# Kernel optimization log

Measured on AMD Instinct MI355X. Metric: run time of the kernel, lower is better.

Reference implementation:

```python
import jax, jax.numpy as jnp
import numpy as np

K, R, D = 200000, 64, 1024
N_IDS = 16384
BITS = 4
GROUP = 32


def group_quantize(w, bits, group_size):
    """Group-wise symmetric fake-quant along the last dim (STE in bwd)."""
    last = w.shape[-1]
    g = min(group_size, last)
    n_groups = last // g
    wg = w.reshape(w.shape[:-1] + (n_groups, g))
    amax = jnp.clip(jnp.max(jnp.abs(wg), axis=-1, keepdims=True), 1e-8, None)
    q_max = (1 << (bits - 1)) - 1  # matches torch `1 << bits - 1` precedence
    scale = amax / q_max
    q = jnp.clip(jnp.round(wg / scale), -q_max, q_max) * scale
    # straight-through estimator: forward = q, backward = identity w.r.t. wg
    wq = wg + jax.lax.stop_gradient(q - wg)
    return wq.reshape(w.shape)


def setup_inputs() -> dict:
    key = jax.random.key(0)
    k1, k2, k3 = jax.random.split(key, 3)
    U = jax.random.normal(k1, (K, R), dtype=jnp.float32)
    B = jax.random.normal(k2, (R, D), dtype=jnp.float32)
    local_ids = jax.random.randint(k3, (N_IDS,), 0, K, dtype=jnp.int64 if jax.config.read('jax_enable_x64') else jnp.int32)
    return {"U": U, "B": B, "local_ids": local_ids}


def reference(U, B, local_ids):
    # row(): quantize ALL of U, gather selected rows, matmul with quantized B
    Uq = group_quantize(U, BITS, min(GROUP, R))   # [K, r]
    Bq = group_quantize(B, BITS, min(GROUP, D))   # [r, d]
    return Uq[local_ids] @ Bq                      # [N, d]
```

## Files before the change

kernel.cpp:

```cpp
#include <hip/hip_runtime.h>


#define R_DIM 64
#define D_DIM 1024
#define N_IDS 16384

#define BM 64
#define BN 128
#define LDS_STRIDE 72
#define OT_STRIDE 132

typedef __attribute__((ext_vector_type(8))) __bf16 bf16x8;
typedef __attribute__((ext_vector_type(4))) float f32x4;

__device__ inline unsigned short f32_to_bf16_rne(float f) {
  union { float f; unsigned int u; } c; c.f = f;
  unsigned int u = c.u;
  u += 0x7fffu + ((u >> 16) & 1u);
  return (unsigned short)(u >> 16);
}

__device__ inline float bf16_bits_to_f32(unsigned short h) {
  union { unsigned int u; float f; } c; c.u = ((unsigned int)h) << 16;
  return c.f;
}

__device__ inline void quant_split(float w, float a, unsigned short* hi, unsigned short* lo) {
  double amax  = fmax((double)a, 1e-8);
  double scale = amax / 7.0;
  double t     = (double)w / scale;
  double q     = fmin(fmax(rint(t), -7.0), 7.0) * scale;
  float qf = (float)q;
  unsigned short h = f32_to_bf16_rne(qf);
  *hi = h;
  *lo = f32_to_bf16_rne(qf - bf16_bits_to_f32(h));
}

__global__ __launch_bounds__(256) void quantB_kernel(
    const float* __restrict__ B,
    unsigned short* __restrict__ BqT_hi, unsigned short* __restrict__ BqT_lo) {
  int e = blockIdx.x * 256 + threadIdx.x;
  int r = e >> 10;
  int c = e & 1023;
  float w = B[e];
  float a = fabsf(w);
  a = fmaxf(a, __shfl_xor(a, 1));
  a = fmaxf(a, __shfl_xor(a, 2));
  a = fmaxf(a, __shfl_xor(a, 4));
  a = fmaxf(a, __shfl_xor(a, 8));
  a = fmaxf(a, __shfl_xor(a, 16));
  unsigned short hi, lo;
  quant_split(w, a, &hi, &lo);
  BqT_hi[c * R_DIM + r] = hi;
  BqT_lo[c * R_DIM + r] = lo;
}

__global__ __launch_bounds__(256) void gemm_kernel(
    const float* __restrict__ U, const int* __restrict__ ids,
    const unsigned short* __restrict__ BqT_hi, const unsigned short* __restrict__ BqT_lo,
    float* __restrict__ out) {
  __shared__ char smem[2 * BN * LDS_STRIDE * 2];
  unsigned short* bt_hi = (unsigned short*)smem;
  unsigned short* bt_lo = bt_hi + BN * LDS_STRIDE;
  float* ot = (float*)smem;

  const int tid  = threadIdx.x;
  const int lane = tid & 63;
  const int wave = tid >> 6;
  const int bx   = blockIdx.x;
  const int nb   = bx & 7;
  const int mb   = bx >> 3;
  const int n0   = nb * BN;

  {
    const uint4* src_hi = (const uint4*)(BqT_hi + (size_t)n0 * R_DIM);
    const uint4* src_lo = (const uint4*)(BqT_lo + (size_t)n0 * R_DIM);
    #pragma unroll
    for (int it = 0; it < 4; ++it) {
      int c = tid + it * 256;
      int row = c >> 3, off = c & 7;
      *(uint4*)&bt_hi[row * LDS_STRIDE + off * 8] = src_hi[c];
      *(uint4*)&bt_lo[row * LDS_STRIDE + off * 8] = src_lo[c];
    }
  }

  const int m0    = mb * BM + wave * 16;
  const int rowid = ids[m0 + (lane & 15)];
  const int koff  = (lane >> 4) * 8;
  const int nlane = lane & 15;
  const float* urow = U + (size_t)rowid * R_DIM;

  bf16x8 afrag_hi[2], afrag_lo[2];
  #pragma unroll
  for (int s = 0; s < 2; ++s) {
    float4 w0 = *(const float4*)(urow + s * 32 + koff);
    float4 w1 = *(const float4*)(urow + s * 32 + koff + 4);
    float wv[8] = {w0.x, w0.y, w0.z, w0.w, w1.x, w1.y, w1.z, w1.w};
    float a = 0.0f;
    #pragma unroll
    for (int j = 0; j < 8; ++j) a = fmaxf(a, fabsf(wv[j]));
    a = fmaxf(a, __shfl_xor(a, 16));
    a = fmaxf(a, __shfl_xor(a, 32));
    union { unsigned short s8[8]; bf16x8 b; } uh, ul;
    #pragma unroll
    for (int j = 0; j < 8; ++j) {
      unsigned short hi, lo;
      quant_split(wv[j], a, &hi, &lo);
      uh.s8[j] = hi;
      ul.s8[j] = lo;
    }
    afrag_hi[s] = uh.b;
    afrag_lo[s] = ul.b;
  }

  __syncthreads();

  f32x4 acc[8];
  #pragma unroll
  for (int nf = 0; nf < 8; ++nf) acc[nf] = (f32x4){0.f, 0.f, 0.f, 0.f};

  #pragma unroll
  for (int nf = 0; nf < 8; ++nf) {
    #pragma unroll
    for (int s = 0; s < 2; ++s) {
      const int boff = (nf * 16 + nlane) * LDS_STRIDE + s * 32 + koff;
      union { uint4 u; bf16x8 b; } bh, bl;
      bh.u = *(const uint4*)&bt_hi[boff];
      bl.u = *(const uint4*)&bt_lo[boff];
      acc[nf] = __builtin_amdgcn_mfma_f32_16x16x32_bf16(afrag_hi[s], bh.b, acc[nf], 0, 0, 0);
      acc[nf] = __builtin_amdgcn_mfma_f32_16x16x32_bf16(afrag_hi[s], bl.b, acc[nf], 0, 0, 0);
      acc[nf] = __builtin_amdgcn_mfma_f32_16x16x32_bf16(afrag_lo[s], bh.b, acc[nf], 0, 0, 0);
    }
  }

  __syncthreads();

  float* w = ot + wave * 16 * OT_STRIDE;
  {
    const int r0 = (lane >> 4) << 2;
    #pragma unroll
    for (int nf = 0; nf < 8; ++nf) {
      #pragma unroll
      for (int i = 0; i < 4; ++i) {
        w[(r0 + i) * OT_STRIDE + nlane + nf * 16] = acc[nf][i];
      }
    }
  }
  #pragma unroll
  for (int j = 0; j < 8; ++j) {
    const int row = j * 2 + (lane >> 5);
    f32x4 v = *(const f32x4*)&w[row * OT_STRIDE + (lane & 31) * 4];
    __builtin_nontemporal_store(v,
        (f32x4*)&out[(size_t)(m0 + row) * D_DIM + n0 + (lane & 31) * 4]);
  }
}

extern "C" void kernel_launch(void* const* d_in, const int* in_sizes, int n_in,
                              void* d_out, int out_size, void* d_ws, size_t ws_size,
                              hipStream_t stream) {
  const float* U   = (const float*)d_in[0];
  const float* B   = (const float*)d_in[1];
  const int*   ids = (const int*)d_in[2];
  float* out = (float*)d_out;

  unsigned short* BqT_hi = (unsigned short*)d_ws;
  unsigned short* BqT_lo = BqT_hi + R_DIM * D_DIM;

  quantB_kernel<<<(R_DIM * D_DIM) / 256, 256, 0, stream>>>(B, BqT_hi, BqT_lo);
  gemm_kernel<<<(N_IDS / BM) * (D_DIM / BN), 256, 0, stream>>>(U, ids, BqT_hi, BqT_lo, out);
}
```

Baseline: 27.29 us.

## Double GEMM M-tile per block, hoist gathered U loads, vectorize B quantization

Each gemm block now covers 128 rows instead of 64, and each wave computes two 16-row fragments. That way every B fragment read from LDS feeds twice as many MFMAs, and the per-block B tile staging is amortized over more output rows. The gathered U row loads are issued before the B tile is copied into LDS, so their global latency overlaps the staging. quantB now processes four elements per thread with a float4 load and shorter shuffle reductions, and the gemm kernel gets a launch-bounds occupancy hint. The trade-off is higher register pressure and half as many blocks in the grid, which could reduce latency hiding in a kernel that is mostly bound by output writes.

```diff
diff --git a/kernel.cpp b/kernel.cpp
--- a/kernel.cpp
+++ b/kernel.cpp
@@ -5,7 +5,7 @@
 #define D_DIM 1024
 #define N_IDS 16384
 
-#define BM 64
+#define BM 128
 #define BN 128
 #define LDS_STRIDE 72
 #define OT_STRIDE 132
@@ -25,11 +25,10 @@
   return c.f;
 }
 
-__device__ inline void quant_split(float w, float a, unsigned short* hi, unsigned short* lo) {
-  double amax  = fmax((double)a, 1e-8);
-  double scale = amax / 7.0;
-  double t     = (double)w / scale;
-  double q     = fmin(fmax(rint(t), -7.0), 7.0) * scale;
+__device__ inline void quant_elem(float w, double scale,
+                                  unsigned short* hi, unsigned short* lo) {
+  double t = (double)w / scale;
+  double q = fmin(fmax(rint(t), -7.0), 7.0) * scale;
   float qf = (float)q;
   unsigned short h = f32_to_bf16_rne(qf);
   *hi = h;
@@ -39,23 +38,27 @@
 __global__ __launch_bounds__(256) void quantB_kernel(
     const float* __restrict__ B,
     unsigned short* __restrict__ BqT_hi, unsigned short* __restrict__ BqT_lo) {
-  int e = blockIdx.x * 256 + threadIdx.x;
-  int r = e >> 10;
-  int c = e & 1023;
-  float w = B[e];
-  float a = fabsf(w);
+  int e4 = blockIdx.x * 256 + threadIdx.x;
+  int e  = e4 * 4;
+  int r  = e >> 10;
+  int c  = e & 1023;
+  float4 w = *(const float4*)(B + e);
+  float a = fmaxf(fmaxf(fabsf(w.x), fabsf(w.y)), fmaxf(fabsf(w.z), fabsf(w.w)));
   a = fmaxf(a, __shfl_xor(a, 1));
   a = fmaxf(a, __shfl_xor(a, 2));
   a = fmaxf(a, __shfl_xor(a, 4));
-  a = fmaxf(a, __shfl_xor(a, 8));
-  a = fmaxf(a, __shfl_xor(a, 16));
-  unsigned short hi, lo;
-  quant_split(w, a, &hi, &lo);
-  BqT_hi[c * R_DIM + r] = hi;
-  BqT_lo[c * R_DIM + r] = lo;
+  double sc = fmax((double)a, 1e-8) / 7.0;
+  float wv[4] = {w.x, w.y, w.z, w.w};
+  #pragma unroll
+  for (int j = 0; j < 4; ++j) {
+    unsigned short hi, lo;
+    quant_elem(wv[j], sc, &hi, &lo);
+    BqT_hi[(c + j) * R_DIM + r] = hi;
+    BqT_lo[(c + j) * R_DIM + r] = lo;
+  }
 }
 
-__global__ __launch_bounds__(256) void gemm_kernel(
+__global__ __launch_bounds__(256, 4) void gemm_kernel(
     const float* __restrict__ U, const int* __restrict__ ids,
     const unsigned short* __restrict__ BqT_hi, const unsigned short* __restrict__ BqT_lo,
     float* __restrict__ out) {
@@ -71,6 +74,20 @@
   const int nb   = bx & 7;
   const int mb   = bx >> 3;
   const int n0   = nb * BN;
+  const int m0b  = mb * BM;
+  const int koff  = (lane >> 4) * 8;
+  const int nlane = lane & 15;
+
+  const float* urow0 = U + (size_t)ids[m0b + wave * 16 + nlane] * R_DIM;
+  const float* urow1 = U + (size_t)ids[m0b + 64 + wave * 16 + nlane] * R_DIM;
+  float4 wr[2][2][2];
+  #pragma unroll
+  for (int s = 0; s < 2; ++s) {
+    wr[0][s][0] = *(const float4*)(urow0 + s * 32 + koff);
+    wr[0][s][1] = *(const float4*)(urow0 + s * 32 + koff + 4);
+    wr[1][s][0] = *(const float4*)(urow1 + s * 32 + koff);
+    wr[1][s][1] = *(const float4*)(urow1 + s * 32 + koff + 4);
+  }
 
   {
     const uint4* src_hi = (const uint4*)(BqT_hi + (size_t)n0 * R_DIM);
@@ -84,40 +101,39 @@
     }
   }
 
-  const int m0    = mb * BM + wave * 16;
-  const int rowid = ids[m0 + (lane & 15)];
-  const int koff  = (lane >> 4) * 8;
-  const int nlane = lane & 15;
-  const float* urow = U + (size_t)rowid * R_DIM;
-
-  bf16x8 afrag_hi[2], afrag_lo[2];
+  bf16x8 ah[2][2], al[2][2];
   #pragma unroll
-  for (int s = 0; s < 2; ++s) {
-    float4 w0 = *(const float4*)(urow + s * 32 + koff);
-    float4 w1 = *(const float4*)(urow + s * 32 + koff + 4);
-    float wv[8] = {w0.x, w0.y, w0.z, w0.w, w1.x, w1.y, w1.z, w1.w};
-    float a = 0.0f;
+  for (int mf = 0; mf < 2; ++mf) {
     #pragma unroll
-    for (int j = 0; j < 8; ++j) a = fmaxf(a, fabsf(wv[j]));
-    a = fmaxf(a, __shfl_xor(a, 16));
-    a = fmaxf(a, __shfl_xor(a, 32));
-    union { unsigned short s8[8]; bf16x8 b; } uh, ul;
-    #pragma unroll
-    for (int j = 0; j < 8; ++j) {
-      unsigned short hi, lo;
-      quant_split(wv[j], a, &hi, &lo);
-      uh.s8[j] = hi;
-      ul.s8[j] = lo;
+    for (int s = 0; s < 2; ++s) {
+      float4 w0 = wr[mf][s][0], w1 = wr[mf][s][1];
+      float wv[8] = {w0.x, w0.y, w0.z, w0.w, w1.x, w1.y, w1.z, w1.w};
+      float a = 0.0f;
+      #pragma unroll
+      for (int j = 0; j < 8; ++j) a = fmaxf(a, fabsf(wv[j]));
+      a = fmaxf(a, __shfl_xor(a, 16));
+      a = fmaxf(a, __shfl_xor(a, 32));
+      double sc = fmax((double)a, 1e-8) / 7.0;
+      union { unsigned short s8[8]; bf16x8 b; } uh, ul;
+      #pragma unroll
+      for (int j = 0; j < 8; ++j) {
+        unsigned short hi, lo;
+        quant_elem(wv[j], sc, &hi, &lo);
+        uh.s8[j] = hi;
+        ul.s8[j] = lo;
+      }
+      ah[mf][s] = uh.b;
+      al[mf][s] = ul.b;
     }
-    afrag_hi[s] = uh.b;
-    afrag_lo[s] = ul.b;
   }
 
   __syncthreads();
 
-  f32x4 acc[8];
+  f32x4 acc[2][8];
   #pragma unroll
-  for (int nf = 0; nf < 8; ++nf) acc[nf] = (f32x4){0.f, 0.f, 0.f, 0.f};
+  for (int mf = 0; mf < 2; ++mf)
+    #pragma unroll
+    for (int nf = 0; nf < 8; ++nf) acc[mf][nf] = (f32x4){0.f, 0.f, 0.f, 0.f};
 
   #pragma unroll
   for (int nf = 0; nf < 8; ++nf) {
@@ -127,31 +143,36 @@
       union { uint4 u; bf16x8 b; } bh, bl;
       bh.u = *(const uint4*)&bt_hi[boff];
       bl.u = *(const uint4*)&bt_lo[boff];
-      acc[nf] = __builtin_amdgcn_mfma_f32_16x16x32_bf16(afrag_hi[s], bh.b, acc[nf], 0, 0, 0);
-      acc[nf] = __builtin_amdgcn_mfma_f32_16x16x32_bf16(afrag_hi[s], bl.b, acc[nf], 0, 0, 0);
-      acc[nf] = __builtin_amdgcn_mfma_f32_16x16x32_bf16(afrag_lo[s], bh.b, acc[nf], 0, 0, 0);
+      #pragma unroll
+      for (int mf = 0; mf < 2; ++mf) {
+        acc[mf][nf] = __builtin_amdgcn_mfma_f32_16x16x32_bf16(ah[mf][s], bh.b, acc[mf][nf], 0, 0, 0);
+        acc[mf][nf] = __builtin_amdgcn_mfma_f32_16x16x32_bf16(ah[mf][s], bl.b, acc[mf][nf], 0, 0, 0);
+        acc[mf][nf] = __builtin_amdgcn_mfma_f32_16x16x32_bf16(al[mf][s], bh.b, acc[mf][nf], 0, 0, 0);
+      }
     }
   }
 
   __syncthreads();
 
-  float* w = ot + wave * 16 * OT_STRIDE;
-  {
+  float* wp = ot + wave * 16 * OT_STRIDE;
+  #pragma unroll
+  for (int mf = 0; mf < 2; ++mf) {
     const int r0 = (lane >> 4) << 2;
     #pragma unroll
     for (int nf = 0; nf < 8; ++nf) {
       #pragma unroll
       for (int i = 0; i < 4; ++i) {
-        w[(r0 + i) * OT_STRIDE + nlane + nf * 16] = acc[nf][i];
+        wp[(r0 + i) * OT_STRIDE + nlane + nf * 16] = acc[mf][nf][i];
       }
     }
-  }
-  #pragma unroll
-  for (int j = 0; j < 8; ++j) {
-    const int row = j * 2 + (lane >> 5);
-    f32x4 v = *(const f32x4*)&w[row * OT_STRIDE + (lane & 31) * 4];
-    __builtin_nontemporal_store(v,
-        (f32x4*)&out[(size_t)(m0 + row) * D_DIM + n0 + (lane & 31) * 4]);
+    const int orow0 = m0b + mf * 64 + wave * 16;
+    #pragma unroll
+    for (int j = 0; j < 8; ++j) {
+      const int row = j * 2 + (lane >> 5);
+      f32x4 v = *(const f32x4*)&wp[row * OT_STRIDE + (lane & 31) * 4];
+      __builtin_nontemporal_store(v,
+          (f32x4*)&out[(size_t)(orow0 + row) * D_DIM + n0 + (lane & 31) * 4]);
+    }
   }
 }
 
@@ -166,6 +187,6 @@
   unsigned short* BqT_hi = (unsigned short*)d_ws;
   unsigned short* BqT_lo = BqT_hi + R_DIM * D_DIM;
 
-  quantB_kernel<<<(R_DIM * D_DIM) / 256, 256, 0, stream>>>(B, BqT_hi, BqT_lo);
+  quantB_kernel<<<(R_DIM * D_DIM) / (256 * 4), 256, 0, stream>>>(B, BqT_hi, BqT_lo);
   gemm_kernel<<<(N_IDS / BM) * (D_DIM / BN), 256, 0, stream>>>(U, ids, BqT_hi, BqT_lo, out);
 }
```

New measurement: 27.47 us. Within noise of the previous version (+0.7%).
